# Optimization experiments

Measured on AMD Instinct MI355X. Metric: run time of the kernel, lower is better.

## Reference

```python
import jax, jax.numpy as jnp
import numpy as np

B, S, D = 1, 2048, 4096
H, KVH, HD = 32, 8, 128
ROPE_THETA = 10000.0


def setup_inputs() -> dict:
    key = jax.random.key(0)
    k1, k2, k3, k4, k5 = jax.random.split(key, 5)
    scale = D ** -0.5
    return {
        "hidden_states": jax.random.normal(k1, (B, S, D), dtype=jnp.float32),
        "position_ids": jnp.arange(S, dtype=jnp.int64).reshape(1, S),
        "Wq": jax.random.normal(k2, (H * HD, D), dtype=jnp.float32) * scale,
        "Wk": jax.random.normal(k3, (KVH * HD, D), dtype=jnp.float32) * scale,
        "Wv": jax.random.normal(k4, (KVH * HD, D), dtype=jnp.float32) * scale,
        "Wo": jax.random.normal(k5, (D, H * HD), dtype=jnp.float32) * scale,
    }


def _rotate_half(x):
    x1, x2 = x[..., : HD // 2], x[..., HD // 2 :]
    return jnp.concatenate((-x2, x1), axis=-1)


def reference(hidden_states, position_ids, Wq, Wk, Wv, Wo):
    b, s, d = hidden_states.shape
    # projections: nn.Linear applies x @ W.T
    q = jnp.einsum("bsd,ed->bse", hidden_states, Wq).reshape(b, s, H, HD).transpose(0, 2, 1, 3)
    k = jnp.einsum("bsd,ed->bse", hidden_states, Wk).reshape(b, s, KVH, HD).transpose(0, 2, 1, 3)
    v = jnp.einsum("bsd,ed->bse", hidden_states, Wv).reshape(b, s, KVH, HD).transpose(0, 2, 1, 3)
    # rotary embedding (default rope: inv_freq = theta^(-2i/d), attention_scaling = 1)
    inv_freq = 1.0 / (ROPE_THETA ** (jnp.arange(0, HD, 2, dtype=jnp.float32) / HD))
    pos = position_ids.astype(jnp.float32)  # [Bp, S]
    freqs = pos[:, :, None] * inv_freq[None, None, :]  # [Bp, S, HD/2]
    emb = jnp.concatenate((freqs, freqs), axis=-1)  # [Bp, S, HD]
    cos = jnp.cos(emb)[:, None, :, :]  # unsqueeze head dim
    sin = jnp.sin(emb)[:, None, :, :]
    q = q * cos + _rotate_half(q) * sin
    k = k * cos + _rotate_half(k) * sin
    # GQA: expand kv heads to match query heads
    groups = H // KVH
    k = jnp.repeat(k, groups, axis=1)
    v = jnp.repeat(v, groups, axis=1)
    # causal attention, scaling = head_dim^-0.5
    scores = jnp.einsum("bhqd,bhkd->bhqk", q, k) * (HD ** -0.5)
    causal = jnp.tril(jnp.ones((s, s), dtype=bool))
    scores = jnp.where(causal[None, None], scores, jnp.finfo(scores.dtype).min)
    attn = jax.nn.softmax(scores, axis=-1)
    out = jnp.einsum("bhqk,bhkd->bhqd", attn, v)
    out = out.transpose(0, 2, 1, 3).reshape(b, s, H * HD)
    return jnp.einsum("bse,de->bsd", out, Wo)
```

## Files before the change

kernel.cpp:

```cpp
#include <hip/hip_runtime.h>
#include <stdint.h>

typedef unsigned short u16;
typedef __attribute__((ext_vector_type(4))) float f32x4;
typedef __attribute__((ext_vector_type(8))) short bf16x8;

static constexpr int S   = 2048;
static constexpr int DM  = 4096;
static constexpr int NH  = 32;
static constexpr int NKV = 8;
static constexpr int HD  = 128;
static constexpr int LDQ = 5120;

__device__ __forceinline__ u16 f2bf(float f) {
    union { float f; unsigned u; } v; v.f = f;
    return (u16)((v.u + 0x7FFFu + ((v.u >> 16) & 1u)) >> 16);
}
__device__ __forceinline__ float bf2f(u16 h) {
    union { unsigned u; float f; } v; v.u = ((unsigned)h) << 16;
    return v.f;
}

__device__ __forceinline__ void mfma16(f32x4& d, bf16x8 a, bf16x8 b) {
    asm("v_mfma_f32_16x16x32_bf16 %0, %1, %2, %0" : "+v"(d) : "v"(a), "v"(b));
}

__device__ __forceinline__ void gload_lds16(const u16* g, u16* lds) {
    __builtin_amdgcn_global_load_lds((__attribute__((address_space(1))) void*)g,
                                     (__attribute__((address_space(3))) void*)lds,
                                     16, 0, 0);
}

__global__ __launch_bounds__(256) void cvt_kernel(const float* __restrict__ in,
                                                  u16* __restrict__ out, int n4) {
    int i = blockIdx.x * blockDim.x + threadIdx.x;
    int stride = gridDim.x * blockDim.x;
    for (; i < n4; i += stride) {
        float4 v = ((const float4*)in)[i];
        ushort4 o;
        o.x = f2bf(v.x); o.y = f2bf(v.y); o.z = f2bf(v.z); o.w = f2bf(v.w);
        ((ushort4*)out)[i] = o;
    }
}

__global__ __launch_bounds__(256) void cvt_qkv(const float* __restrict__ Wq,
                                               const float* __restrict__ Wk,
                                               const float* __restrict__ Wv,
                                               u16* __restrict__ out) {
    const int n4 = 6144 * 4096 / 4;
    int i = blockIdx.x * blockDim.x + threadIdx.x;
    int stride = gridDim.x * blockDim.x;
    for (; i < n4; i += stride) {
        float4 v;
        if (i < 4194304)       v = ((const float4*)Wq)[i];
        else if (i < 5242880)  v = ((const float4*)Wk)[i - 4194304];
        else                   v = ((const float4*)Wv)[i - 5242880];
        ushort4 o;
        o.x = f2bf(v.x); o.y = f2bf(v.y); o.z = f2bf(v.z); o.w = f2bf(v.w);
        ((ushort4*)out)[i] = o;
    }
}

__global__ __launch_bounds__(256) void rope_table_kernel(float2* __restrict__ tbl) {
    int i = blockIdx.x * blockDim.x + threadIdx.x;
    if (i >= S * 64) return;
    int p = i >> 6, j = i & 63;
    float inv = powf(10000.0f, -(float)j / 64.0f);
    float a = (float)p * inv;
    tbl[i] = make_float2(cosf(a), sinf(a));
}

__global__ __launch_bounds__(256) void rope_kernel(u16* __restrict__ X,
                                                   const float2* __restrict__ tbl,
                                                   int nh, int ld, float scale) {
    int i = blockIdx.x * blockDim.x + threadIdx.x;
    int total = S * nh * 64;
    if (i >= total) return;
    int dd = i & 63;
    int t2 = i >> 6;
    int hh = t2 % nh;
    int s  = t2 / nh;
    size_t base = (size_t)s * ld + (size_t)hh * HD + dd;
    float x1 = bf2f(X[base]);
    float x2 = bf2f(X[base + 64]);
    float2 cs = tbl[(s << 6) + dd];
    X[base]      = f2bf((x1 * cs.x - x2 * cs.y) * scale);
    X[base + 64] = f2bf((x2 * cs.x + x1 * cs.y) * scale);
}

template<int MODE>
__global__ __launch_bounds__(256)
void gemm_bt(const u16* __restrict__ A, const u16* __restrict__ Bt,
             void* __restrict__ Cv, int M, int N, int K, int lda, int ldb, int ldc) {
    __shared__ u16 Al[128][64];
    __shared__ u16 Bl[128][64];
    const int t = threadIdx.x;
    const int w = t >> 6, l = t & 63;
    const int r16 = l & 15, g4 = l >> 4;
    const int m0 = blockIdx.y * 128, n0 = blockIdx.x * 128;
    const int wr = (w >> 1) * 64, wc = (w & 1) * 64;

    f32x4 acc[4][4];
#pragma unroll
    for (int i = 0; i < 4; ++i)
#pragma unroll
        for (int j = 0; j < 4; ++j) acc[i][j] = f32x4{0.f, 0.f, 0.f, 0.f};

    for (int kt = 0; kt < K; kt += 64) {
#pragma unroll
        for (int i = 0; i < 4; ++i) {
            int c = i * 256 + t;
            gload_lds16(A + (size_t)(m0 + (c >> 3)) * lda + kt + ((c & 7) << 3),
                        &Al[0][0] + ((i * 256 + w * 64) << 3));
        }
#pragma unroll
        for (int i = 0; i < 4; ++i) {
            int c = i * 256 + t;
            gload_lds16(Bt + (size_t)(n0 + (c >> 3)) * ldb + kt + ((c & 7) << 3),
                        &Bl[0][0] + ((i * 256 + w * 64) << 3));
        }
        asm volatile("s_waitcnt vmcnt(0)" ::: "memory");
        __syncthreads();

#pragma unroll
        for (int kk = 0; kk < 2; ++kk) {
            bf16x8 af[4], bfr[4];
#pragma unroll
            for (int mi = 0; mi < 4; ++mi)
                af[mi] = *(const bf16x8*)&Al[wr + mi * 16 + r16][kk * 32 + g4 * 8];
#pragma unroll
            for (int ni = 0; ni < 4; ++ni)
                bfr[ni] = *(const bf16x8*)&Bl[wc + ni * 16 + r16][kk * 32 + g4 * 8];
#pragma unroll
            for (int mi = 0; mi < 4; ++mi)
#pragma unroll
                for (int ni = 0; ni < 4; ++ni)
                    mfma16(acc[mi][ni], af[mi], bfr[ni]);
        }
        __syncthreads();
    }

    const int rb = g4 * 4;
#pragma unroll
    for (int mi = 0; mi < 4; ++mi) {
#pragma unroll
        for (int ni = 0; ni < 4; ++ni) {
            const int n = n0 + wc + ni * 16 + r16;
            const int mbase = m0 + wr + mi * 16 + rb;
            float* C = (float*)Cv;
#pragma unroll
            for (int j = 0; j < 4; ++j)
                C[(size_t)(mbase + j) * ldc + n] = acc[mi][ni][j];
        }
    }
}

__global__ __launch_bounds__(256)
void gemm_qkv(const u16* __restrict__ A, const u16* __restrict__ Bt,
              u16* __restrict__ Cqk, u16* __restrict__ Vt) {
    __shared__ u16 Al[128][64];
    __shared__ u16 Bl[128][64];
    const int t = threadIdx.x;
    const int w = t >> 6, l = t & 63;
    const int r16 = l & 15, g4 = l >> 4;
    const int m0 = blockIdx.y * 128, n0 = blockIdx.x * 128;
    const int wr = (w >> 1) * 64, wc = (w & 1) * 64;

    f32x4 acc[4][4];
#pragma unroll
    for (int i = 0; i < 4; ++i)
#pragma unroll
        for (int j = 0; j < 4; ++j) acc[i][j] = f32x4{0.f, 0.f, 0.f, 0.f};

    for (int kt = 0; kt < DM; kt += 64) {
#pragma unroll
        for (int i = 0; i < 4; ++i) {
            int c = i * 256 + t;
            gload_lds16(A + (size_t)(m0 + (c >> 3)) * DM + kt + ((c & 7) << 3),
                        &Al[0][0] + ((i * 256 + w * 64) << 3));
        }
#pragma unroll
        for (int i = 0; i < 4; ++i) {
            int c = i * 256 + t;
            gload_lds16(Bt + (size_t)(n0 + (c >> 3)) * DM + kt + ((c & 7) << 3),
                        &Bl[0][0] + ((i * 256 + w * 64) << 3));
        }
        asm volatile("s_waitcnt vmcnt(0)" ::: "memory");
        __syncthreads();

#pragma unroll
        for (int kk = 0; kk < 2; ++kk) {
            bf16x8 af[4], bfr[4];
#pragma unroll
            for (int mi = 0; mi < 4; ++mi)
                af[mi] = *(const bf16x8*)&Al[wr + mi * 16 + r16][kk * 32 + g4 * 8];
#pragma unroll
            for (int ni = 0; ni < 4; ++ni)
                bfr[ni] = *(const bf16x8*)&Bl[wc + ni * 16 + r16][kk * 32 + g4 * 8];
#pragma unroll
            for (int mi = 0; mi < 4; ++mi)
#pragma unroll
                for (int ni = 0; ni < 4; ++ni)
                    mfma16(acc[mi][ni], af[mi], bfr[ni]);
        }
        __syncthreads();
    }

    const int rb = g4 * 4;
    if (n0 < 5120) {
#pragma unroll
        for (int mi = 0; mi < 4; ++mi)
#pragma unroll
            for (int ni = 0; ni < 4; ++ni) {
                const int n = n0 + wc + ni * 16 + r16;
                const int mbase = m0 + wr + mi * 16 + rb;
#pragma unroll
                for (int j = 0; j < 4; ++j)
                    Cqk[(size_t)(mbase + j) * LDQ + n] = f2bf(acc[mi][ni][j]);
            }
    } else {
#pragma unroll
        for (int mi = 0; mi < 4; ++mi)
#pragma unroll
            for (int ni = 0; ni < 4; ++ni) {
                const int n = n0 + wc + ni * 16 + r16 - 5120;
                const int mbase = m0 + wr + mi * 16 + rb;
                ushort4 v;
                v.x = f2bf(acc[mi][ni][0]); v.y = f2bf(acc[mi][ni][1]);
                v.z = f2bf(acc[mi][ni][2]); v.w = f2bf(acc[mi][ni][3]);
                *(ushort4*)&Vt[(size_t)n * S + mbase] = v;
            }
    }
}

__global__ __launch_bounds__(256, 2)
void attn_fwd(const u16* __restrict__ QK, const u16* __restrict__ Vt,
              u16* __restrict__ O) {
    __shared__ u16 Kl[2][64 * 128];
    __shared__ u16 Vl[2][128 * 64];
    __shared__ u16 Pl[4 * 16 * 64];

    const int t = threadIdx.x;
    const int w = t >> 6, l = t & 63;
    const int r16 = l & 15, g4 = l >> 4;
    const int h = blockIdx.y;
    const int kvh = h >> 2;
    const int p = blockIdx.x;
    const int q0A = p * 64, q0B = (31 - p) * 64;
    const int ntA = p + 1, ntB = 32 - p;

    const u16* Kg = QK + 4096 + kvh * HD;
    const u16* Vg = Vt + (size_t)(kvh * HD) * S;
    u16* Pb = &Pl[w * 1024];

    bf16x8 qfA[4], qfB[4];
    {
        const u16* Qg = QK + h * HD;
        const size_t qrA = (size_t)(q0A + w * 16 + r16) * LDQ;
        const size_t qrB = (size_t)(q0B + w * 16 + r16) * LDQ;
#pragma unroll
        for (int kg = 0; kg < 4; ++kg) {
            qfA[kg] = *(const bf16x8*)&Qg[qrA + kg * 32 + g4 * 8];
            qfB[kg] = *(const bf16x8*)&Qg[qrB + kg * 32 + g4 * 8];
        }
    }

    f32x4 accA[8], accB[8];
    float mA[4], lA[4], mB[4], lB[4];
#pragma unroll
    for (int i = 0; i < 8; ++i) { accA[i] = f32x4{0,0,0,0}; accB[i] = f32x4{0,0,0,0}; }
#pragma unroll
    for (int j = 0; j < 4; ++j) { mA[j] = -3.0e38f; lA[j] = 0.f; mB[j] = -3.0e38f; lB[j] = 0.f; }

    auto stage = [&](int tk, int b) {
        const int kv0 = tk * 64;
#pragma unroll
        for (int i = 0; i < 4; ++i) {
            int c = i * 256 + t;
            int r = c >> 4, s = (c & 15) ^ (r & 7);
            gload_lds16(Kg + (size_t)(kv0 + r) * LDQ + (s << 3),
                        &Kl[b][0] + ((i * 256 + w * 64) << 3));
        }
#pragma unroll
        for (int i = 0; i < 4; ++i) {
            int c = i * 256 + t;
            int r = c >> 3, s = (c & 7) ^ (r & 7);
            gload_lds16(Vg + (size_t)r * S + kv0 + (s << 3),
                        &Vl[b][0] + ((i * 256 + w * 64) << 3));
        }
    };

    auto compute = [&](f32x4 (&acco)[8], float (&mrun)[4], float (&lrun)[4],
                       const bf16x8 (&qf)[4], int q0, int tk, bool maskit, int b) {
        const int kv0 = tk * 64;
        const u16* Kb = &Kl[b][0];
        const u16* Vb = &Vl[b][0];

        f32x4 sc[4];
#pragma unroll
        for (int ni = 0; ni < 4; ++ni) sc[ni] = f32x4{0,0,0,0};
#pragma unroll
        for (int kg = 0; kg < 4; ++kg) {
#pragma unroll
            for (int ni = 0; ni < 4; ++ni) {
                int row = ni * 16 + r16;
                int bb = (row * 256 + kg * 64 + g4 * 16) ^ ((row & 7) << 4);
                bf16x8 kf = *(const bf16x8*)((const char*)Kb + bb);
                mfma16(sc[ni], qf[kg], kf);
            }
        }

        float vmax[4];
        bool grow = false;
#pragma unroll
        for (int j = 0; j < 4; ++j) {
            if (maskit) {
                const int qg = q0 + w * 16 + g4 * 4 + j;
#pragma unroll
                for (int ni = 0; ni < 4; ++ni)
                    if (kv0 + ni * 16 + r16 > qg) sc[ni][j] = -3.0e38f;
            }
            float v = fmaxf(fmaxf(sc[0][j], sc[1][j]), fmaxf(sc[2][j], sc[3][j]));
            v = fmaxf(v, __shfl_xor(v, 1, 16));
            v = fmaxf(v, __shfl_xor(v, 2, 16));
            v = fmaxf(v, __shfl_xor(v, 4, 16));
            v = fmaxf(v, __shfl_xor(v, 8, 16));
            vmax[j] = v;
            grow = grow || (v > mrun[j] + 11.5f);
        }
        float fac[4] = {1.f, 1.f, 1.f, 1.f};
        if (__any(grow)) {
#pragma unroll
            for (int j = 0; j < 4; ++j) {
                float nm = fmaxf(mrun[j], vmax[j]);
                fac[j] = exp2f(mrun[j] - nm);
                mrun[j] = nm;
            }
#pragma unroll
            for (int i = 0; i < 8; ++i)
#pragma unroll
                for (int j = 0; j < 4; ++j) acco[i][j] *= fac[j];
        }
#pragma unroll
        for (int j = 0; j < 4; ++j) {
            float p0 = exp2f(sc[0][j] - mrun[j]);
            float p1 = exp2f(sc[1][j] - mrun[j]);
            float p2 = exp2f(sc[2][j] - mrun[j]);
            float p3 = exp2f(sc[3][j] - mrun[j]);
            sc[0][j] = p0; sc[1][j] = p1; sc[2][j] = p2; sc[3][j] = p3;
            float s2 = (p0 + p1) + (p2 + p3);
            s2 += __shfl_xor(s2, 1, 16);
            s2 += __shfl_xor(s2, 2, 16);
            s2 += __shfl_xor(s2, 4, 16);
            s2 += __shfl_xor(s2, 8, 16);
            lrun[j] = lrun[j] * fac[j] + s2;
        }

#pragma unroll
        for (int ni = 0; ni < 4; ++ni)
#pragma unroll
            for (int j = 0; j < 4; ++j) {
                int row = g4 * 4 + j;
                int bb = (row * 128 + ((ni * 16 + r16) << 1)) ^ ((row & 7) << 4);
                *(u16*)((char*)Pb + bb) = f2bf(sc[ni][j]);
            }
        asm volatile("s_waitcnt lgkmcnt(0)" ::: "memory");
        __builtin_amdgcn_sched_barrier(0);

        int pb0 = (r16 * 128 + g4 * 16) ^ ((r16 & 7) << 4);
        bf16x8 pf0 = *(const bf16x8*)((const char*)Pb + pb0);
        bf16x8 pf1 = *(const bf16x8*)((const char*)Pb + (pb0 ^ 64));
#pragma unroll
        for (int ni = 0; ni < 8; ++ni) {
            int row = ni * 16 + r16;
            int bb = (row * 128 + g4 * 16) ^ ((row & 7) << 4);
            bf16x8 v0 = *(const bf16x8*)((const char*)Vb + bb);
            mfma16(acco[ni], pf0, v0);
            bf16x8 v1 = *(const bf16x8*)((const char*)Vb + (bb ^ 64));
            mfma16(acco[ni], pf1, v1);
        }
    };

    auto epilogue = [&](f32x4 (&acco)[8], float (&lrun)[4], int q0) {
        float rl[4];
#pragma unroll
        for (int j = 0; j < 4; ++j) rl[j] = 1.0f / lrun[j];
#pragma unroll
        for (int ni = 0; ni < 8; ++ni)
#pragma unroll
            for (int j = 0; j < 4; ++j) {
                const int qg = q0 + w * 16 + g4 * 4 + j;
                O[(size_t)qg * DM + h * HD + ni * 16 + r16] = f2bf(acco[ni][j] * rl[j]);
            }
    };

    stage(0, 0);
    asm volatile("s_waitcnt vmcnt(0)" ::: "memory");
    __syncthreads();
    int buf = 0;

    for (int tk = 0; tk < ntA; ++tk) {
        if (tk + 1 < ntA) stage(tk + 1, buf ^ 1);
        else              stage(0, buf ^ 1);
        compute(accA, mA, lA, qfA, q0A, tk, tk == ntA - 1, buf);
        asm volatile("s_waitcnt vmcnt(0)" ::: "memory");
        __syncthreads();
        buf ^= 1;
    }
    epilogue(accA, lA, q0A);

    for (int tk = 0; tk < ntB; ++tk) {
        if (tk + 1 < ntB) stage(tk + 1, buf ^ 1);
        compute(accB, mB, lB, qfB, q0B, tk, tk == ntB - 1, buf);
        asm volatile("s_waitcnt vmcnt(0)" ::: "memory");
        __syncthreads();
        buf ^= 1;
    }
    epilogue(accB, lB, q0B);
}

extern "C" void kernel_launch(void* const* d_in, const int* in_sizes, int n_in,
                              void* d_out, int out_size, void* d_ws, size_t ws_size,
                              hipStream_t stream) {
    const float* X  = (const float*)d_in[0];
    const float* Wq = (const float*)d_in[2];
    const float* Wk = (const float*)d_in[3];
    const float* Wv = (const float*)d_in[4];
    const float* Wo = (const float*)d_in[5];

    char* ws = (char*)d_ws;
    u16*    Xbf  = (u16*)(ws + 0);
    u16*    Wqkv = (u16*)(ws + 16777216);
    u16*    Wobf = (u16*)(ws + 67108864);
    u16*    QKb  = (u16*)(ws + 100663296);
    u16*    Vtbf = (u16*)(ws + 121634816);
    u16*    Obf  = (u16*)(ws + 125829120);
    float2* tbl  = (float2*)(ws + 142606336);
    if (ws_size < 143654912ull) return;

    dim3 blk(256);

    cvt_kernel<<<2048, blk, 0, stream>>>(X,  Xbf,  S * DM / 4);
    cvt_qkv<<<2048, blk, 0, stream>>>(Wq, Wk, Wv, Wqkv);
    cvt_kernel<<<2048, blk, 0, stream>>>(Wo, Wobf, DM * DM / 4);
    rope_table_kernel<<<(S * 64 + 255) / 256, blk, 0, stream>>>(tbl);

    gemm_qkv<<<dim3(48, 16), blk, 0, stream>>>(Xbf, Wqkv, QKb, Vtbf);

    rope_kernel<<<(S * NH * 64 + 255) / 256, blk, 0, stream>>>(
        QKb, tbl, NH, LDQ, 0.08838834764831845f * 1.4426950408889634f);
    rope_kernel<<<(S * NKV * 64 + 255) / 256, blk, 0, stream>>>(
        QKb + 4096, tbl, NKV, LDQ, 1.0f);

    attn_fwd<<<dim3(16, NH), blk, 0, stream>>>(QKb, Vtbf, Obf);

    gemm_bt<1><<<dim3(DM / 128, S / 128), blk, 0, stream>>>(
        Obf, Wobf, d_out, S, DM, DM, DM, DM, DM);
}
```

Baseline: 386.1 us.

## Replace GEMMs with double-buffered 256x256 eight-wave kernel and raise MFMA priority

Replaces the two 128x128 single-buffered GEMM kernels with one 256x256-tile, 512-thread kernel. It double-buffers swizzled LDS tiles, prefetches the next k-tile in three chunks interleaved with four MFMA sub-blocks, and remaps block IDs for L2 locality. s_setprio is also raised around the MFMA sections in attention. The aim is to hide global-load latency, cut LDS bank conflicts and raise per-block data reuse. The cost is fewer blocks (192 and 128 on many CUs) and heavy register and LDS use, which may hurt occupancy and tail balance.

```diff
diff --git a/kernel.cpp b/kernel.cpp
--- a/kernel.cpp
+++ b/kernel.cpp
@@ -11,6 +11,8 @@
 static constexpr int NKV = 8;
 static constexpr int HD  = 128;
 static constexpr int LDQ = 5120;
+
+template<int V> struct ic { static constexpr int v = V; };
 
 __device__ __forceinline__ u16 f2bf(float f) {
     union { float f; unsigned u; } v; v.f = f;
@@ -88,147 +90,166 @@
     X[base + 64] = f2bf((x2 * cs.x + x1 * cs.y) * scale);
 }
 
-template<int MODE>
-__global__ __launch_bounds__(256)
-void gemm_bt(const u16* __restrict__ A, const u16* __restrict__ Bt,
-             void* __restrict__ Cv, int M, int N, int K, int lda, int ldb, int ldc) {
-    __shared__ u16 Al[128][64];
-    __shared__ u16 Bl[128][64];
+template<int MODE, int NBX>
+__global__ __launch_bounds__(512, 2)
+void gemm8(const u16* __restrict__ A, const u16* __restrict__ Bt,
+           u16* __restrict__ Cqk, u16* __restrict__ Vt, float* __restrict__ Cf) {
+    __shared__ u16 LA[2][256 * 64];
+    __shared__ u16 LB[2][256 * 64];
     const int t = threadIdx.x;
     const int w = t >> 6, l = t & 63;
     const int r16 = l & 15, g4 = l >> 4;
-    const int m0 = blockIdx.y * 128, n0 = blockIdx.x * 128;
-    const int wr = (w >> 1) * 64, wc = (w & 1) * 64;
-
-    f32x4 acc[4][4];
-#pragma unroll
-    for (int i = 0; i < 4; ++i)
+    const int wm = w >> 2, wn = w & 3;
+
+    const int id = blockIdx.x;
+    const int sw = (id & 7) * NBX + (id >> 3);
+    const int bx = sw % NBX, by = sw / NBX;
+    const int m0 = by * 256, n0 = bx * 256;
+
+    auto stB = [&](int kt, int b) {
+#pragma unroll
+        for (int i = 0; i < 4; ++i) {
+            int c = i * 512 + t;
+            int r = c >> 3, s = (c & 7) ^ (r & 7);
+            gload_lds16(Bt + (size_t)(n0 + r) * DM + kt + (s << 3),
+                        &LB[b][0] + ((i * 512 + w * 64) << 3));
+        }
+    };
+    auto stA = [&](int kt, int b, int sub) {
+#pragma unroll
+        for (int i = 0; i < 2; ++i) {
+            int c = i * 1024 + sub * 512 + t;
+            int r = c >> 3, s = (c & 7) ^ (r & 7);
+            gload_lds16(A + (size_t)(m0 + r) * DM + kt + (s << 3),
+                        &LA[b][0] + ((i * 1024 + sub * 512 + w * 64) << 3));
+        }
+    };
+
+    bf16x8 a[8], bq[8];
+    f32x4 acc[8][4];
+#pragma unroll
+    for (int i = 0; i < 8; ++i)
 #pragma unroll
         for (int j = 0; j < 4; ++j) acc[i][j] = f32x4{0.f, 0.f, 0.f, 0.f};
 
-    for (int kt = 0; kt < K; kt += 64) {
-#pragma unroll
-        for (int i = 0; i < 4; ++i) {
-            int c = i * 256 + t;
-            gload_lds16(A + (size_t)(m0 + (c >> 3)) * lda + kt + ((c & 7) << 3),
-                        &Al[0][0] + ((i * 256 + w * 64) << 3));
-        }
-#pragma unroll
-        for (int i = 0; i < 4; ++i) {
-            int c = i * 256 + t;
-            gload_lds16(Bt + (size_t)(n0 + (c >> 3)) * ldb + kt + ((c & 7) << 3),
-                        &Bl[0][0] + ((i * 256 + w * 64) << 3));
-        }
-        asm volatile("s_waitcnt vmcnt(0)" ::: "memory");
-        __syncthreads();
-
-#pragma unroll
-        for (int kk = 0; kk < 2; ++kk) {
-            bf16x8 af[4], bfr[4];
-#pragma unroll
-            for (int mi = 0; mi < 4; ++mi)
-                af[mi] = *(const bf16x8*)&Al[wr + mi * 16 + r16][kk * 32 + g4 * 8];
-#pragma unroll
-            for (int ni = 0; ni < 4; ++ni)
-                bfr[ni] = *(const bf16x8*)&Bl[wc + ni * 16 + r16][kk * 32 + g4 * 8];
-#pragma unroll
-            for (int mi = 0; mi < 4; ++mi)
-#pragma unroll
-                for (int ni = 0; ni < 4; ++ni)
-                    mfma16(acc[mi][ni], af[mi], bfr[ni]);
-        }
-        __syncthreads();
-    }
-
-    const int rb = g4 * 4;
-#pragma unroll
-    for (int mi = 0; mi < 4; ++mi) {
-#pragma unroll
-        for (int ni = 0; ni < 4; ++ni) {
-            const int n = n0 + wc + ni * 16 + r16;
-            const int mbase = m0 + wr + mi * 16 + rb;
-            float* C = (float*)Cv;
-#pragma unroll
-            for (int j = 0; j < 4; ++j)
-                C[(size_t)(mbase + j) * ldc + n] = acc[mi][ni][j];
-        }
-    }
-}
-
-__global__ __launch_bounds__(256)
-void gemm_qkv(const u16* __restrict__ A, const u16* __restrict__ Bt,
-              u16* __restrict__ Cqk, u16* __restrict__ Vt) {
-    __shared__ u16 Al[128][64];
-    __shared__ u16 Bl[128][64];
-    const int t = threadIdx.x;
-    const int w = t >> 6, l = t & 63;
-    const int r16 = l & 15, g4 = l >> 4;
-    const int m0 = blockIdx.y * 128, n0 = blockIdx.x * 128;
-    const int wr = (w >> 1) * 64, wc = (w & 1) * 64;
-
-    f32x4 acc[4][4];
-#pragma unroll
-    for (int i = 0; i < 4; ++i)
-#pragma unroll
-        for (int j = 0; j < 4; ++j) acc[i][j] = f32x4{0.f, 0.f, 0.f, 0.f};
-
-    for (int kt = 0; kt < DM; kt += 64) {
-#pragma unroll
-        for (int i = 0; i < 4; ++i) {
-            int c = i * 256 + t;
-            gload_lds16(A + (size_t)(m0 + (c >> 3)) * DM + kt + ((c & 7) << 3),
-                        &Al[0][0] + ((i * 256 + w * 64) << 3));
-        }
-#pragma unroll
-        for (int i = 0; i < 4; ++i) {
-            int c = i * 256 + t;
-            gload_lds16(Bt + (size_t)(n0 + (c >> 3)) * DM + kt + ((c & 7) << 3),
-                        &Bl[0][0] + ((i * 256 + w * 64) << 3));
-        }
-        asm volatile("s_waitcnt vmcnt(0)" ::: "memory");
-        __syncthreads();
-
-#pragma unroll
-        for (int kk = 0; kk < 2; ++kk) {
-            bf16x8 af[4], bfr[4];
-#pragma unroll
-            for (int mi = 0; mi < 4; ++mi)
-                af[mi] = *(const bf16x8*)&Al[wr + mi * 16 + r16][kk * 32 + g4 * 8];
-#pragma unroll
-            for (int ni = 0; ni < 4; ++ni)
-                bfr[ni] = *(const bf16x8*)&Bl[wc + ni * 16 + r16][kk * 32 + g4 * 8];
-#pragma unroll
-            for (int mi = 0; mi < 4; ++mi)
-#pragma unroll
-                for (int ni = 0; ni < 4; ++ni)
-                    mfma16(acc[mi][ni], af[mi], bfr[ni]);
-        }
-        __syncthreads();
-    }
-
-    const int rb = g4 * 4;
-    if (n0 < 5120) {
+    auto rdA = [&](const u16* base, auto MHt) {
+        constexpr int MH = decltype(MHt)::v;
 #pragma unroll
         for (int mi = 0; mi < 4; ++mi)
 #pragma unroll
+            for (int kk = 0; kk < 2; ++kk) {
+                int r = wm * 128 + MH * 64 + mi * 16 + r16;
+                int bb = (r * 128 + kk * 64 + g4 * 16) ^ ((r & 7) << 4);
+                a[mi * 2 + kk] = *(const bf16x8*)((const char*)base + bb);
+            }
+    };
+    auto rdB = [&](const u16* base, auto NHt) {
+        constexpr int NH_ = decltype(NHt)::v;
+#pragma unroll
+        for (int ni = 0; ni < 2; ++ni)
+#pragma unroll
+            for (int kk = 0; kk < 2; ++kk) {
+                int r = wn * 64 + (NH_ * 2 + ni) * 16 + r16;
+                int bb = (r * 128 + kk * 64 + g4 * 16) ^ ((r & 7) << 4);
+                bq[(NH_ * 2 + ni) * 2 + kk] = *(const bf16x8*)((const char*)base + bb);
+            }
+    };
+    auto mm = [&](auto MHt, auto NHt) {
+        constexpr int MH = decltype(MHt)::v;
+        constexpr int NH_ = decltype(NHt)::v;
+        __builtin_amdgcn_s_setprio(1);
+#pragma unroll
+        for (int mi = 0; mi < 4; ++mi)
+#pragma unroll
+            for (int ni = 0; ni < 2; ++ni)
+#pragma unroll
+                for (int kk = 0; kk < 2; ++kk)
+                    mfma16(acc[MH * 4 + mi][NH_ * 2 + ni],
+                           a[mi * 2 + kk], bq[(NH_ * 2 + ni) * 2 + kk]);
+        __builtin_amdgcn_s_setprio(0);
+    };
+
+    stB(0, 0); stA(0, 0, 0); stA(0, 0, 1);
+    asm volatile("s_waitcnt vmcnt(0)" ::: "memory");
+    __builtin_amdgcn_s_barrier();
+    asm volatile("" ::: "memory");
+
+    for (int tk = 0; tk < 64; ++tk) {
+        const int b = tk & 1;
+        const u16* Ab = &LA[b][0];
+        const u16* Bb = &LB[b][0];
+        const int ktn = (tk + 1) * 64;
+        const bool pf = (tk + 1 < 64);
+
+        rdA(Ab, ic<0>{}); rdB(Bb, ic<0>{});
+        if (pf) stB(ktn, b ^ 1);
+        __builtin_amdgcn_s_barrier();
+        asm volatile("s_waitcnt lgkmcnt(0)" ::: "memory");
+        __builtin_amdgcn_sched_barrier(0);
+        mm(ic<0>{}, ic<0>{});
+        __builtin_amdgcn_s_barrier();
+        asm volatile("" ::: "memory");
+
+        rdB(Bb, ic<1>{});
+        if (pf) stA(ktn, b ^ 1, 0);
+        __builtin_amdgcn_s_barrier();
+        asm volatile("s_waitcnt lgkmcnt(0)" ::: "memory");
+        __builtin_amdgcn_sched_barrier(0);
+        mm(ic<0>{}, ic<1>{});
+        asm volatile("s_waitcnt vmcnt(6)" ::: "memory");
+        __builtin_amdgcn_s_barrier();
+        asm volatile("" ::: "memory");
+
+        rdA(Ab, ic<1>{});
+        if (pf) stA(ktn, b ^ 1, 1);
+        __builtin_amdgcn_s_barrier();
+        asm volatile("s_waitcnt lgkmcnt(0)" ::: "memory");
+        __builtin_amdgcn_sched_barrier(0);
+        mm(ic<1>{}, ic<1>{});
+        __builtin_amdgcn_s_barrier();
+        asm volatile("" ::: "memory");
+
+        mm(ic<1>{}, ic<0>{});
+        asm volatile("s_waitcnt vmcnt(2)" ::: "memory");
+        __builtin_amdgcn_s_barrier();
+        asm volatile("" ::: "memory");
+    }
+
+    if constexpr (MODE == 0) {
+        if (n0 < 5120) {
+#pragma unroll
+            for (int fi = 0; fi < 8; ++fi)
+#pragma unroll
+                for (int ni = 0; ni < 4; ++ni) {
+                    const int row = m0 + wm * 128 + fi * 16 + g4 * 4;
+                    const int col = n0 + wn * 64 + ni * 16 + r16;
+#pragma unroll
+                    for (int j = 0; j < 4; ++j)
+                        Cqk[(size_t)(row + j) * LDQ + col] = f2bf(acc[fi][ni][j]);
+                }
+        } else {
+#pragma unroll
+            for (int fi = 0; fi < 8; ++fi)
+#pragma unroll
+                for (int ni = 0; ni < 4; ++ni) {
+                    const int row = m0 + wm * 128 + fi * 16 + g4 * 4;
+                    const int col = n0 + wn * 64 + ni * 16 + r16 - 5120;
+                    ushort4 v4;
+                    v4.x = f2bf(acc[fi][ni][0]); v4.y = f2bf(acc[fi][ni][1]);
+                    v4.z = f2bf(acc[fi][ni][2]); v4.w = f2bf(acc[fi][ni][3]);
+                    *(ushort4*)&Vt[(size_t)col * S + row] = v4;
+                }
+        }
+    } else {
+#pragma unroll
+        for (int fi = 0; fi < 8; ++fi)
+#pragma unroll
             for (int ni = 0; ni < 4; ++ni) {
-                const int n = n0 + wc + ni * 16 + r16;
-                const int mbase = m0 + wr + mi * 16 + rb;
+                const int row = m0 + wm * 128 + fi * 16 + g4 * 4;
+                const int col = n0 + wn * 64 + ni * 16 + r16;
 #pragma unroll
                 for (int j = 0; j < 4; ++j)
-                    Cqk[(size_t)(mbase + j) * LDQ + n] = f2bf(acc[mi][ni][j]);
-            }
-    } else {
-#pragma unroll
-        for (int mi = 0; mi < 4; ++mi)
-#pragma unroll
-            for (int ni = 0; ni < 4; ++ni) {
-                const int n = n0 + wc + ni * 16 + r16 - 5120;
-                const int mbase = m0 + wr + mi * 16 + rb;
-                ushort4 v;
-                v.x = f2bf(acc[mi][ni][0]); v.y = f2bf(acc[mi][ni][1]);
-                v.z = f2bf(acc[mi][ni][2]); v.w = f2bf(acc[mi][ni][3]);
-                *(ushort4*)&Vt[(size_t)n * S + mbase] = v;
+                    Cf[(size_t)(row + j) * DM + col] = acc[fi][ni][j];
             }
     }
 }
@@ -299,6 +320,7 @@
         f32x4 sc[4];
 #pragma unroll
         for (int ni = 0; ni < 4; ++ni) sc[ni] = f32x4{0,0,0,0};
+        __builtin_amdgcn_s_setprio(1);
 #pragma unroll
         for (int kg = 0; kg < 4; ++kg) {
 #pragma unroll
@@ -309,6 +331,7 @@
                 mfma16(sc[ni], qf[kg], kf);
             }
         }
+        __builtin_amdgcn_s_setprio(0);
 
         float vmax[4];
         bool grow = false;
@@ -370,6 +393,7 @@
         int pb0 = (r16 * 128 + g4 * 16) ^ ((r16 & 7) << 4);
         bf16x8 pf0 = *(const bf16x8*)((const char*)Pb + pb0);
         bf16x8 pf1 = *(const bf16x8*)((const char*)Pb + (pb0 ^ 64));
+        __builtin_amdgcn_s_setprio(1);
 #pragma unroll
         for (int ni = 0; ni < 8; ++ni) {
             int row = ni * 16 + r16;
@@ -379,6 +403,7 @@
             bf16x8 v1 = *(const bf16x8*)((const char*)Vb + (bb ^ 64));
             mfma16(acco[ni], pf1, v1);
         }
+        __builtin_amdgcn_s_setprio(0);
     };
 
     auto epilogue = [&](f32x4 (&acco)[8], float (&lrun)[4], int q0) {
@@ -445,7 +470,7 @@
     cvt_kernel<<<2048, blk, 0, stream>>>(Wo, Wobf, DM * DM / 4);
     rope_table_kernel<<<(S * 64 + 255) / 256, blk, 0, stream>>>(tbl);
 
-    gemm_qkv<<<dim3(48, 16), blk, 0, stream>>>(Xbf, Wqkv, QKb, Vtbf);
+    gemm8<0, 24><<<dim3(192), dim3(512), 0, stream>>>(Xbf, Wqkv, QKb, Vtbf, nullptr);
 
     rope_kernel<<<(S * NH * 64 + 255) / 256, blk, 0, stream>>>(
         QKb, tbl, NH, LDQ, 0.08838834764831845f * 1.4426950408889634f);
@@ -454,6 +479,6 @@
 
     attn_fwd<<<dim3(16, NH), blk, 0, stream>>>(QKb, Vtbf, Obf);
 
-    gemm_bt<1><<<dim3(DM / 128, S / 128), blk, 0, stream>>>(
-        Obf, Wobf, d_out, S, DM, DM, DM, DM, DM);
-}
+    gemm8<1, 16><<<dim3(128), dim3(512), 0, stream>>>(Obf, Wobf, nullptr, nullptr,
+                                                      (float*)d_out);
+}
```

Measured after the change: 449.5 us. 16.4% more time.

## Swizzle GEMM LDS tiles and merge attention query tiles into 512-thread blocks

Applied to the files above, without the earlier changes.

Applies an XOR swizzle to the LDS staging of both GEMM kernels so the MFMA fragment reads avoid bank conflicts. The attention kernel moves to 512 threads (8 waves) per block, each handling 128-query pair tiles. The two paired query tiles now share one K/V stream, so each staged KV tile is reused by both halves instead of being loaded twice, and the causal mask is computed per wave. s_setprio hints are added around the MFMA sections. This halves the attention grid and raises register and LDS pressure per block.

```diff
diff --git a/kernel.cpp b/kernel.cpp
--- a/kernel.cpp
+++ b/kernel.cpp
@@ -88,12 +88,11 @@
     X[base + 64] = f2bf((x2 * cs.x + x1 * cs.y) * scale);
 }
 
-template<int MODE>
 __global__ __launch_bounds__(256)
 void gemm_bt(const u16* __restrict__ A, const u16* __restrict__ Bt,
-             void* __restrict__ Cv, int M, int N, int K, int lda, int ldb, int ldc) {
-    __shared__ u16 Al[128][64];
-    __shared__ u16 Bl[128][64];
+             float* __restrict__ C, int M, int N, int K, int lda, int ldb, int ldc) {
+    __shared__ u16 Al[128 * 64];
+    __shared__ u16 Bl[128 * 64];
     const int t = threadIdx.x;
     const int w = t >> 6, l = t & 63;
     const int r16 = l & 15, g4 = l >> 4;
@@ -110,14 +109,16 @@
 #pragma unroll
         for (int i = 0; i < 4; ++i) {
             int c = i * 256 + t;
-            gload_lds16(A + (size_t)(m0 + (c >> 3)) * lda + kt + ((c & 7) << 3),
-                        &Al[0][0] + ((i * 256 + w * 64) << 3));
+            int r = c >> 3, s = (c & 7) ^ (r & 7);
+            gload_lds16(A + (size_t)(m0 + r) * lda + kt + (s << 3),
+                        Al + ((i * 256 + w * 64) << 3));
         }
 #pragma unroll
         for (int i = 0; i < 4; ++i) {
             int c = i * 256 + t;
-            gload_lds16(Bt + (size_t)(n0 + (c >> 3)) * ldb + kt + ((c & 7) << 3),
-                        &Bl[0][0] + ((i * 256 + w * 64) << 3));
+            int r = c >> 3, s = (c & 7) ^ (r & 7);
+            gload_lds16(Bt + (size_t)(n0 + r) * ldb + kt + (s << 3),
+                        Bl + ((i * 256 + w * 64) << 3));
         }
         asm volatile("s_waitcnt vmcnt(0)" ::: "memory");
         __syncthreads();
@@ -126,11 +127,17 @@
         for (int kk = 0; kk < 2; ++kk) {
             bf16x8 af[4], bfr[4];
 #pragma unroll
-            for (int mi = 0; mi < 4; ++mi)
-                af[mi] = *(const bf16x8*)&Al[wr + mi * 16 + r16][kk * 32 + g4 * 8];
-#pragma unroll
-            for (int ni = 0; ni < 4; ++ni)
-                bfr[ni] = *(const bf16x8*)&Bl[wc + ni * 16 + r16][kk * 32 + g4 * 8];
+            for (int mi = 0; mi < 4; ++mi) {
+                int r = wr + mi * 16 + r16;
+                af[mi] = *(const bf16x8*)((const char*)Al +
+                          ((r * 128 + kk * 64 + g4 * 16) ^ ((r & 7) << 4)));
+            }
+#pragma unroll
+            for (int ni = 0; ni < 4; ++ni) {
+                int r = wc + ni * 16 + r16;
+                bfr[ni] = *(const bf16x8*)((const char*)Bl +
+                           ((r * 128 + kk * 64 + g4 * 16) ^ ((r & 7) << 4)));
+            }
 #pragma unroll
             for (int mi = 0; mi < 4; ++mi)
 #pragma unroll
@@ -142,24 +149,22 @@
 
     const int rb = g4 * 4;
 #pragma unroll
-    for (int mi = 0; mi < 4; ++mi) {
+    for (int mi = 0; mi < 4; ++mi)
 #pragma unroll
         for (int ni = 0; ni < 4; ++ni) {
             const int n = n0 + wc + ni * 16 + r16;
             const int mbase = m0 + wr + mi * 16 + rb;
-            float* C = (float*)Cv;
 #pragma unroll
             for (int j = 0; j < 4; ++j)
                 C[(size_t)(mbase + j) * ldc + n] = acc[mi][ni][j];
         }
-    }
 }
 
 __global__ __launch_bounds__(256)
 void gemm_qkv(const u16* __restrict__ A, const u16* __restrict__ Bt,
               u16* __restrict__ Cqk, u16* __restrict__ Vt) {
-    __shared__ u16 Al[128][64];
-    __shared__ u16 Bl[128][64];
+    __shared__ u16 Al[128 * 64];
+    __shared__ u16 Bl[128 * 64];
     const int t = threadIdx.x;
     const int w = t >> 6, l = t & 63;
     const int r16 = l & 15, g4 = l >> 4;
@@ -176,14 +181,16 @@
 #pragma unroll
         for (int i = 0; i < 4; ++i) {
             int c = i * 256 + t;
-            gload_lds16(A + (size_t)(m0 + (c >> 3)) * DM + kt + ((c & 7) << 3),
-                        &Al[0][0] + ((i * 256 + w * 64) << 3));
+            int r = c >> 3, s = (c & 7) ^ (r & 7);
+            gload_lds16(A + (size_t)(m0 + r) * DM + kt + (s << 3),
+                        Al + ((i * 256 + w * 64) << 3));
         }
 #pragma unroll
         for (int i = 0; i < 4; ++i) {
             int c = i * 256 + t;
-            gload_lds16(Bt + (size_t)(n0 + (c >> 3)) * DM + kt + ((c & 7) << 3),
-                        &Bl[0][0] + ((i * 256 + w * 64) << 3));
+            int r = c >> 3, s = (c & 7) ^ (r & 7);
+            gload_lds16(Bt + (size_t)(n0 + r) * DM + kt + (s << 3),
+                        Bl + ((i * 256 + w * 64) << 3));
         }
         asm volatile("s_waitcnt vmcnt(0)" ::: "memory");
         __syncthreads();
@@ -192,11 +199,17 @@
         for (int kk = 0; kk < 2; ++kk) {
             bf16x8 af[4], bfr[4];
 #pragma unroll
-            for (int mi = 0; mi < 4; ++mi)
-                af[mi] = *(const bf16x8*)&Al[wr + mi * 16 + r16][kk * 32 + g4 * 8];
-#pragma unroll
-            for (int ni = 0; ni < 4; ++ni)
-                bfr[ni] = *(const bf16x8*)&Bl[wc + ni * 16 + r16][kk * 32 + g4 * 8];
+            for (int mi = 0; mi < 4; ++mi) {
+                int r = wr + mi * 16 + r16;
+                af[mi] = *(const bf16x8*)((const char*)Al +
+                          ((r * 128 + kk * 64 + g4 * 16) ^ ((r & 7) << 4)));
+            }
+#pragma unroll
+            for (int ni = 0; ni < 4; ++ni) {
+                int r = wc + ni * 16 + r16;
+                bfr[ni] = *(const bf16x8*)((const char*)Bl +
+                           ((r * 128 + kk * 64 + g4 * 16) ^ ((r & 7) << 4)));
+            }
 #pragma unroll
             for (int mi = 0; mi < 4; ++mi)
 #pragma unroll
@@ -225,20 +238,20 @@
             for (int ni = 0; ni < 4; ++ni) {
                 const int n = n0 + wc + ni * 16 + r16 - 5120;
                 const int mbase = m0 + wr + mi * 16 + rb;
-                ushort4 v;
-                v.x = f2bf(acc[mi][ni][0]); v.y = f2bf(acc[mi][ni][1]);
-                v.z = f2bf(acc[mi][ni][2]); v.w = f2bf(acc[mi][ni][3]);
-                *(ushort4*)&Vt[(size_t)n * S + mbase] = v;
-            }
-    }
-}
-
-__global__ __launch_bounds__(256, 2)
+                ushort4 v4;
+                v4.x = f2bf(acc[mi][ni][0]); v4.y = f2bf(acc[mi][ni][1]);
+                v4.z = f2bf(acc[mi][ni][2]); v4.w = f2bf(acc[mi][ni][3]);
+                *(ushort4*)&Vt[(size_t)n * S + mbase] = v4;
+            }
+    }
+}
+
+__global__ __launch_bounds__(512, 2)
 void attn_fwd(const u16* __restrict__ QK, const u16* __restrict__ Vt,
               u16* __restrict__ O) {
     __shared__ u16 Kl[2][64 * 128];
     __shared__ u16 Vl[2][128 * 64];
-    __shared__ u16 Pl[4 * 16 * 64];
+    __shared__ u16 Pl[8 * 16 * 64];
 
     const int t = threadIdx.x;
     const int w = t >> 6, l = t & 63;
@@ -246,8 +259,8 @@
     const int h = blockIdx.y;
     const int kvh = h >> 2;
     const int p = blockIdx.x;
-    const int q0A = p * 64, q0B = (31 - p) * 64;
-    const int ntA = p + 1, ntB = 32 - p;
+    const int q0A = p * 128, q0B = (15 - p) * 128;
+    const int ntA = 2 * p + 2, ntB = 32 - 2 * p;
 
     const u16* Kg = QK + 4096 + kvh * HD;
     const u16* Vg = Vt + (size_t)(kvh * HD) * S;
@@ -275,30 +288,32 @@
     auto stage = [&](int tk, int b) {
         const int kv0 = tk * 64;
 #pragma unroll
-        for (int i = 0; i < 4; ++i) {
-            int c = i * 256 + t;
+        for (int i = 0; i < 2; ++i) {
+            int c = i * 512 + t;
             int r = c >> 4, s = (c & 15) ^ (r & 7);
             gload_lds16(Kg + (size_t)(kv0 + r) * LDQ + (s << 3),
-                        &Kl[b][0] + ((i * 256 + w * 64) << 3));
-        }
-#pragma unroll
-        for (int i = 0; i < 4; ++i) {
-            int c = i * 256 + t;
+                        &Kl[b][0] + ((i * 512 + w * 64) << 3));
+        }
+#pragma unroll
+        for (int i = 0; i < 2; ++i) {
+            int c = i * 512 + t;
             int r = c >> 3, s = (c & 7) ^ (r & 7);
             gload_lds16(Vg + (size_t)r * S + kv0 + (s << 3),
-                        &Vl[b][0] + ((i * 256 + w * 64) << 3));
+                        &Vl[b][0] + ((i * 512 + w * 64) << 3));
         }
     };
 
     auto compute = [&](f32x4 (&acco)[8], float (&mrun)[4], float (&lrun)[4],
-                       const bf16x8 (&qf)[4], int q0, int tk, bool maskit, int b) {
+                       const bf16x8 (&qf)[4], int q0, int tk, int b) {
         const int kv0 = tk * 64;
+        const bool maskit = (kv0 + 63 > q0 + (w << 4));
         const u16* Kb = &Kl[b][0];
         const u16* Vb = &Vl[b][0];
 
         f32x4 sc[4];
 #pragma unroll
         for (int ni = 0; ni < 4; ++ni) sc[ni] = f32x4{0,0,0,0};
+        __builtin_amdgcn_s_setprio(1);
 #pragma unroll
         for (int kg = 0; kg < 4; ++kg) {
 #pragma unroll
@@ -309,6 +324,7 @@
                 mfma16(sc[ni], qf[kg], kf);
             }
         }
+        __builtin_amdgcn_s_setprio(0);
 
         float vmax[4];
         bool grow = false;
@@ -370,6 +386,7 @@
         int pb0 = (r16 * 128 + g4 * 16) ^ ((r16 & 7) << 4);
         bf16x8 pf0 = *(const bf16x8*)((const char*)Pb + pb0);
         bf16x8 pf1 = *(const bf16x8*)((const char*)Pb + (pb0 ^ 64));
+        __builtin_amdgcn_s_setprio(1);
 #pragma unroll
         for (int ni = 0; ni < 8; ++ni) {
             int row = ni * 16 + r16;
@@ -379,6 +396,7 @@
             bf16x8 v1 = *(const bf16x8*)((const char*)Vb + (bb ^ 64));
             mfma16(acco[ni], pf1, v1);
         }
+        __builtin_amdgcn_s_setprio(0);
     };
 
     auto epilogue = [&](f32x4 (&acco)[8], float (&lrun)[4], int q0) {
@@ -399,23 +417,15 @@
     __syncthreads();
     int buf = 0;
 
-    for (int tk = 0; tk < ntA; ++tk) {
-        if (tk + 1 < ntA) stage(tk + 1, buf ^ 1);
-        else              stage(0, buf ^ 1);
-        compute(accA, mA, lA, qfA, q0A, tk, tk == ntA - 1, buf);
+    for (int tk = 0; tk < ntB; ++tk) {
+        if (tk + 1 < ntB) stage(tk + 1, buf ^ 1);
+        compute(accB, mB, lB, qfB, q0B, tk, buf);
+        if (tk < ntA) compute(accA, mA, lA, qfA, q0A, tk, buf);
         asm volatile("s_waitcnt vmcnt(0)" ::: "memory");
         __syncthreads();
         buf ^= 1;
     }
     epilogue(accA, lA, q0A);
-
-    for (int tk = 0; tk < ntB; ++tk) {
-        if (tk + 1 < ntB) stage(tk + 1, buf ^ 1);
-        compute(accB, mB, lB, qfB, q0B, tk, tk == ntB - 1, buf);
-        asm volatile("s_waitcnt vmcnt(0)" ::: "memory");
-        __syncthreads();
-        buf ^= 1;
-    }
     epilogue(accB, lB, q0B);
 }
 
@@ -452,8 +462,8 @@
     rope_kernel<<<(S * NKV * 64 + 255) / 256, blk, 0, stream>>>(
         QKb + 4096, tbl, NKV, LDQ, 1.0f);
 
-    attn_fwd<<<dim3(16, NH), blk, 0, stream>>>(QKb, Vtbf, Obf);
-
-    gemm_bt<1><<<dim3(DM / 128, S / 128), blk, 0, stream>>>(
-        Obf, Wobf, d_out, S, DM, DM, DM, DM, DM);
-}
+    attn_fwd<<<dim3(8, NH), dim3(512), 0, stream>>>(QKb, Vtbf, Obf);
+
+    gemm_bt<<<dim3(DM / 128, S / 128), blk, 0, stream>>>(
+        Obf, Wobf, (float*)d_out, S, DM, DM, DM, DM, DM);
+}
```

Result: faster. 358.2 us (-7.2%).
